# Optimization experiments

Measured on AMD Instinct MI355X. Metric: run time of the kernel, lower is better.

## Reference

```python
import jax, jax.numpy as jnp
import numpy as np

D = 512          # hidden_dim
H_HEADS = 8
DH = D // H_HEADS  # 64
L = 6            # n_layers
P = 8            # patch size
KT = 3           # temporal kernel
Z_DIM = 32
FILM_SCALE = 0.5
ROPE_BASE = 10000.0
EPS = 1e-5


def layer_norm(x, g, b):
    mu = x.mean(-1, keepdims=True)
    var = ((x - mu) ** 2).mean(-1, keepdims=True)
    return (x - mu) * jax.lax.rsqrt(var + EPS) * g + b


def rotate_half(x):
    x1, x2 = jnp.split(x, 2, axis=-1)
    return jnp.concatenate([-x2, x1], axis=-1)


def rope_time(T, dtype):
    half = DH // 2
    inv_freq = ROPE_BASE ** (-(jnp.arange(half, dtype=dtype) / half))  # (half,)
    angles = jnp.arange(T, dtype=dtype)[:, None] * inv_freq[None, :]   # (T, half)
    sin = jnp.concatenate([jnp.sin(angles), jnp.sin(angles)], -1)      # (T, DH)
    cos = jnp.concatenate([jnp.cos(angles), jnp.cos(angles)], -1)
    return sin, cos


def setup_inputs() -> dict:
    key = jax.random.key(0)
    ks = iter(jax.random.split(key, 64))
    n = lambda shape, s=0.02: jax.random.normal(next(ks), shape, jnp.float32) * s
    inp = {
        "x": jax.random.normal(next(ks), (16, 32, 3, 64, 64), jnp.float32),
        "z": jax.random.normal(next(ks), (16, 32, Z_DIM), jnp.float32),
        # tokenizer: CausalConv3d (kt,ph,pw)=(3,8,8), stride (1,8,8)
        "conv_w": n((D, 3, KT, P, P)),
        "conv_b": jnp.zeros((D,), jnp.float32),
        "tok_g": jnp.ones((D,), jnp.float32),
        "tok_b": jnp.zeros((D,), jnp.float32),
        # FiLM from z -> (gamma, beta)
        "film_w": n((Z_DIM, 2 * D)),
        "film_b": jnp.zeros((2 * D,), jnp.float32),
        # transformer blocks (stacked over L)
        "ln1_g": jnp.ones((L, D), jnp.float32), "ln1_b": jnp.zeros((L, D), jnp.float32),
        "kqv_w": n((L, D, 3 * D)), "kqv_b": jnp.zeros((L, 3 * D), jnp.float32),
        "proj_w": n((L, D, D)), "proj_b": jnp.zeros((L, D), jnp.float32),
        "ln2_g": jnp.ones((L, D), jnp.float32), "ln2_b": jnp.zeros((L, D), jnp.float32),
        "mlp_w1": n((L, D, 4 * D)), "mlp_b1": jnp.zeros((L, 4 * D), jnp.float32),
        "mlp_w2": n((L, 4 * D, D)), "mlp_b2": jnp.zeros((L, D), jnp.float32),
        "rs_attn": jnp.full((L,), 0.5, jnp.float32),
        "rs_mlp": jnp.full((L,), 0.5, jnp.float32),
        # scoring head
        "head_g": jnp.ones((D,), jnp.float32), "head_b": jnp.zeros((D,), jnp.float32),
        "head_w": n((D, 1)), "head_bias": jnp.zeros((1,), jnp.float32),
    }
    return inp


def _forward(x, z, conv_w, conv_b, tok_g, tok_b, film_w, film_b,
             ln1_g, ln1_b, kqv_w, kqv_b, proj_w, proj_b, ln2_g, ln2_b,
             mlp_w1, mlp_b1, mlp_w2, mlp_b2, rs_attn, rs_mlp,
             head_g, head_b, head_w, head_bias):
    B, T, C, Himg, Wimg = x.shape
    # ---- SpatialTemporalTokenizer: causal Conv3d (pad time on past only) ----
    xc = jnp.transpose(x, (0, 2, 1, 3, 4))  # [B,C,T,H,W]
    y = jax.lax.conv_general_dilated(
        xc, conv_w, window_strides=(1, P, P),
        padding=[(KT - 1, 0), (0, 0), (0, 0)],
        dimension_numbers=("NCDHW", "OIDHW", "NCDHW"))
    y = y + conv_b[None, :, None, None, None]          # [B,D,T,Hn,Wn]
    Hn, Wn = y.shape[3], y.shape[4]
    tok = jnp.transpose(y, (0, 2, 3, 4, 1)).reshape(B, T, Hn * Wn, D)
    tok = layer_norm(tok, tok_g, tok_b)                 # [B,T,N,D]
    # ---- FiLM conditioning from z ----
    gb = z @ film_w + film_b                            # [B,T,2D]
    gamma, beta = jnp.split(gb, 2, axis=-1)
    tok = (1.0 + FILM_SCALE * gamma)[:, :, None, :] * tok + (FILM_SCALE * beta)[:, :, None, :]
    # ---- spatial pooling -> temporal sequence ----
    h = tok.mean(axis=2)                                # [B,T,D]
    # ---- transformer stack (causal, time RoPE, pre-LN, gated residuals) ----
    sin_t, cos_t = rope_time(T, h.dtype)                # (T, DH)
    causal = jnp.tril(jnp.ones((T, T), bool))
    neg_inf = jnp.finfo(h.dtype).min
    for i in range(L):
        xi = layer_norm(h, ln1_g[i], ln1_b[i])
        kqv = xi @ kqv_w[i] + kqv_b[i]                  # [B,T,3D]
        k, q, v = jnp.split(kqv, 3, axis=-1)            # torch chunk order: k,q,v
        sh = lambda t: t.reshape(B, T, H_HEADS, DH).transpose(0, 2, 1, 3)  # [B,h,T,d]
        q, k, v = sh(q), sh(k), sh(v)
        q = q * cos_t + rotate_half(q) * sin_t
        k = k * cos_t + rotate_half(k) * sin_t
        att = jnp.einsum("bhqd,bhkd->bhqk", q, k) / np.sqrt(DH)
        att = jnp.where(causal[None, None], att, neg_inf)
        att = jax.nn.softmax(att, axis=-1)
        yv = jnp.einsum("bhqk,bhkd->bhqd", att, v)
        yv = yv.transpose(0, 2, 1, 3).reshape(B, T, D)
        attn_out = yv @ proj_w[i] + proj_b[i]
        h = h + rs_attn[i] * attn_out
        x2 = layer_norm(h, ln2_g[i], ln2_b[i])
        m = jax.nn.gelu(x2 @ mlp_w1[i] + mlp_b1[i], approximate=False) @ mlp_w2[i] + mlp_b2[i]
        h = h + rs_mlp[i] * m
    # ---- per-timestep score head ----
    h = layer_norm(h, head_g, head_b)
    score = (h @ head_w + head_bias)[..., 0]            # [B,T]
    return score


def reference(x, z, conv_w, conv_b, tok_g, tok_b, film_w, film_b,
              ln1_g, ln1_b, kqv_w, kqv_b, proj_w, proj_b, ln2_g, ln2_b,
              mlp_w1, mlp_b1, mlp_w2, mlp_b2, rs_attn, rs_mlp,
              head_g, head_b, head_w, head_bias):
    return _forward(x, z, conv_w, conv_b, tok_g, tok_b, film_w, film_b,
                    ln1_g, ln1_b, kqv_w, kqv_b, proj_w, proj_b, ln2_g, ln2_b,
                    mlp_w1, mlp_b1, mlp_w2, mlp_b2, rs_attn, rs_mlp,
                    head_g, head_b, head_w, head_bias)
```

## Files before the change

kernel.cpp:

```cpp
#include <hip/hip_runtime.h>
#include <math.h>

#define EPS 1e-5f

typedef __attribute__((ext_vector_type(8))) short short8;
typedef __attribute__((ext_vector_type(4))) float f32x4;

__device__ __forceinline__ short f2bf(float f) {
    unsigned u = __float_as_uint(f);
    u += 0x7fffu + ((u >> 16) & 1u);
    return (short)(u >> 16);
}
__device__ __forceinline__ float bf2f(short s) {
    return __uint_as_float(((unsigned)(unsigned short)s) << 16);
}
__device__ __forceinline__ void async16(const void* g, void* l) {
    __builtin_amdgcn_global_load_lds(
        (const __attribute__((address_space(1))) unsigned*)g,
        (__attribute__((address_space(3))) unsigned*)l, 16, 0, 0);
}

__device__ __forceinline__ float block_reduce_sum_256(float v, float* red) {
    #pragma unroll
    for (int o = 32; o > 0; o >>= 1) v += __shfl_down(v, o, 64);
    __syncthreads();
    if ((threadIdx.x & 63) == 0) red[threadIdx.x >> 6] = v;
    __syncthreads();
    return red[0] + red[1] + red[2] + red[3];
}

__global__ __launch_bounds__(256) void prep_misc(
    const float* __restrict__ z, const float* __restrict__ fw,
    const float* __restrict__ fb, float* __restrict__ gb,
    const float* __restrict__ conv_w, short* __restrict__ wbf,
    const float* __restrict__ x, short* __restrict__ xbf) {
    __shared__ float zs[32];
    int bi = blockIdx.x, tid = threadIdx.x;
    if (bi < 512) {
        if (tid < 32) zs[tid] = z[bi * 32 + tid];
        __syncthreads();
        for (int j = tid; j < 1024; j += 256) {
            float acc = fb[j];
            #pragma unroll
            for (int k = 0; k < 32; k++) acc = fmaf(zs[k], fw[k * 1024 + j], acc);
            gb[bi * 1024 + j] = acc;
        }
    } else if (bi < 1664) {
        int i = (bi - 512) * 256 + tid;
        wbf[i] = f2bf(conv_w[i]);
    } else {
        int i = (bi - 1664) * 256 + tid;
        float4 a = *(const float4*)(x + (size_t)i * 8);
        float4 b = *(const float4*)(x + (size_t)i * 8 + 4);
        short8 o = {f2bf(a.x), f2bf(a.y), f2bf(a.z), f2bf(a.w),
                    f2bf(b.x), f2bf(b.y), f2bf(b.z), f2bf(b.w)};
        *(short8*)(xbf + (size_t)i * 8) = o;
    }
}

__global__ __launch_bounds__(256) void prep_tcast(
    const float* __restrict__ kqv_w, short* __restrict__ kqvT,
    const float* __restrict__ proj_w, short* __restrict__ projT,
    const float* __restrict__ mlp_w1, short* __restrict__ mlp1T,
    const float* __restrict__ mlp_w2, short* __restrict__ mlp2T) {
    __shared__ float tile[32][33];
    int bi = blockIdx.x;
    const float* src; short* dst; int NT, K, N, rel;
    if (bi < 4608)       { src = kqv_w;  dst = kqvT;  NT = 48; K = 512;  N = 1536; rel = bi; }
    else if (bi < 6144)  { src = proj_w; dst = projT; NT = 16; K = 512;  N = 512;  rel = bi - 4608; }
    else if (bi < 12288) { src = mlp_w1; dst = mlp1T; NT = 64; K = 512;  N = 2048; rel = bi - 6144; }
    else                 { src = mlp_w2; dst = mlp2T; NT = 16; K = 2048; N = 512;  rel = bi - 12288; }
    int per = NT * (K / 32);
    int layer = rel / per, r2 = rel - layer * per;
    int nt = r2 % NT, kt = r2 / NT;
    src += (size_t)layer * K * N;
    dst += (size_t)layer * N * K;
    int n0 = nt * 32, k0 = kt * 32;
    int lx = threadIdx.x & 31, ly = threadIdx.x >> 5;
    #pragma unroll
    for (int i = 0; i < 32; i += 8)
        tile[ly + i][lx] = src[(size_t)(k0 + ly + i) * N + n0 + lx];
    __syncthreads();
    int kp = threadIdx.x & 15, nn = threadIdx.x >> 4;
    #pragma unroll
    for (int i = 0; i < 2; i++) {
        int row = nn + i * 16;
        short2 o = {f2bf(tile[kp * 2][row]), f2bf(tile[kp * 2 + 1][row])};
        *(short2*)(dst + (size_t)(n0 + row) * K + k0 + kp * 2) = o;
    }
}

__global__ __launch_bounds__(256, 2) void conv_fused(
    const short* __restrict__ xbf, const short* __restrict__ wbf,
    const float* __restrict__ cb, const float* __restrict__ tg,
    const float* __restrict__ tb, const float* __restrict__ gb,
    float* __restrict__ h) {
    __shared__ short As[64 * 32];
    __shared__ short Bs[512 * 32];
    __shared__ float redsum[4][64], redss[4][64];
    __shared__ float mu_s[64], inv_s[64];
    int bt = blockIdx.x, b = bt >> 5, t = bt & 31;
    int tid = threadIdx.x;
    int wave = tid >> 6, lane = tid & 63, quad = lane >> 4, l16 = lane & 15;

    int rowA = tid >> 2;
    int cA = (tid & 3) ^ ((rowA >> 1) & 3);
    int hn = rowA >> 3, wn2 = rowA & 7;
    long long baseA = (((long long)(b * 32 + t - 2) * 3) << 12)
                      + (long long)(hn * 8) * 64 + wn2 * 8;

    f32x4 acc[4][8];
    #pragma unroll
    for (int mt = 0; mt < 4; mt++)
        #pragma unroll
        for (int nt = 0; nt < 8; nt++) acc[mt][nt] = (f32x4){0.f, 0.f, 0.f, 0.f};

    for (int k0 = 0; k0 < 576; k0 += 32) {
        #pragma unroll
        for (int e = 0; e < 8; e++) {
            int s = e * 256 + tid;
            int n = s >> 2;
            int c = (s & 3) ^ ((n >> 1) & 3);
            async16(wbf + (size_t)n * 576 + k0 + c * 8, Bs + s * 8);
        }
        {
            int ks = (k0 >> 3) + cA;
            int ch = (ks >= 24) + (ks >= 48);
            int r = ks - ch * 24;
            int kt = r >> 3, ph = r & 7;
            short8 v8 = (short8){0, 0, 0, 0, 0, 0, 0, 0};
            if (t + kt >= 2)
                v8 = *(const short8*)(xbf + baseA
                        + ((long long)(kt * 3 + ch) << 12) + ph * 64);
            *(short8*)(As + tid * 8) = v8;
        }
        __syncthreads();
        short8 af[4], bf[8];
        #pragma unroll
        for (int mt = 0; mt < 4; mt++) {
            int row = mt * 16 + l16;
            int pc = quad ^ ((row >> 1) & 3);
            af[mt] = *(const short8*)(As + row * 32 + pc * 8);
        }
        #pragma unroll
        for (int nt = 0; nt < 8; nt++) {
            int row = wave * 128 + nt * 16 + l16;
            int pc = quad ^ ((row >> 1) & 3);
            bf[nt] = *(const short8*)(Bs + row * 32 + pc * 8);
        }
        #pragma unroll
        for (int mt = 0; mt < 4; mt++)
            #pragma unroll
            for (int nt = 0; nt < 8; nt++)
                acc[mt][nt] = __builtin_amdgcn_mfma_f32_16x16x32_bf16(
                    af[mt], bf[nt], acc[mt][nt], 0, 0, 0);
        __syncthreads();
    }

    float cbn[8], tgn[8], tbn[8], Gn[8], Ben[8];
    #pragma unroll
    for (int nt = 0; nt < 8; nt++) {
        int n = wave * 128 + nt * 16 + l16;
        cbn[nt] = cb[n]; tgn[nt] = tg[n]; tbn[nt] = tb[n];
        Gn[nt]  = 1.f + 0.5f * gb[bt * 1024 + n];
        Ben[nt] = 0.5f * gb[bt * 1024 + 512 + n];
    }
    #pragma unroll
    for (int mt = 0; mt < 4; mt++)
        #pragma unroll
        for (int reg = 0; reg < 4; reg++) {
            float s = 0.f, ss = 0.f;
            #pragma unroll
            for (int nt = 0; nt < 8; nt++) {
                float v = acc[mt][nt][reg] + cbn[nt];
                s += v; ss += v * v;
            }
            #pragma unroll
            for (int o = 1; o < 16; o <<= 1) {
                s  += __shfl_xor(s, o, 64);
                ss += __shfl_xor(ss, o, 64);
            }
            if (l16 == 0) {
                int m = mt * 16 + quad * 4 + reg;
                redsum[wave][m] = s; redss[wave][m] = ss;
            }
        }
    __syncthreads();
    if (tid < 64) {
        float S  = redsum[0][tid] + redsum[1][tid] + redsum[2][tid] + redsum[3][tid];
        float SS = redss[0][tid] + redss[1][tid] + redss[2][tid] + redss[3][tid];
        float mu = S * (1.f / 512.f);
        float var = SS * (1.f / 512.f) - mu * mu;
        mu_s[tid] = mu; inv_s[tid] = rsqrtf(var + EPS);
    }
    __syncthreads();
    float hacc[8] = {0.f, 0.f, 0.f, 0.f, 0.f, 0.f, 0.f, 0.f};
    #pragma unroll
    for (int mt = 0; mt < 4; mt++)
        #pragma unroll
        for (int reg = 0; reg < 4; reg++) {
            int m = mt * 16 + quad * 4 + reg;
            float mu = mu_s[m], inv = inv_s[m];
            #pragma unroll
            for (int nt = 0; nt < 8; nt++) {
                float v = acc[mt][nt][reg] + cbn[nt];
                hacc[nt] += (v - mu) * inv;
            }
        }
    #pragma unroll
    for (int nt = 0; nt < 8; nt++) {
        hacc[nt] += __shfl_xor(hacc[nt], 16, 64);
        hacc[nt] += __shfl_xor(hacc[nt], 32, 64);
    }
    if (quad == 0)
        #pragma unroll
        for (int nt = 0; nt < 8; nt++) {
            int n = wave * 128 + nt * 16 + l16;
            h[bt * 512 + n] = Gn[nt] * (tgn[nt] * (hacc[nt] * (1.f / 64.f)) + tbn[nt])
                              + Ben[nt];
        }
}

__global__ __launch_bounds__(256) void attn_fused(
    const float* __restrict__ hsrc, const float* __restrict__ lng,
    const float* __restrict__ lnb, const short* __restrict__ Bw,
    const float* __restrict__ bias, short* __restrict__ yv) {
    __shared__ char smem[57344] __attribute__((aligned(16)));
    __shared__ float mu_s[32], inv_s[32];
    short* As = (short*)smem;
    short* Bs = (short*)(smem + 32768);
    float (*qs)[64] = (float(*)[64])(smem);
    float (*ks)[64] = (float(*)[64])(smem + 8192);
    float (*vs)[64] = (float(*)[64])(smem + 16384);
    float (*qr)[64] = (float(*)[64])(smem + 24576);
    float (*kr)[64] = (float(*)[64])(smem + 32768);
    float (*att)[32] = (float(*)[32])(smem + 40960);
    int blk = blockIdx.x, b = blk >> 3, hh = blk & 7;
    int tid = threadIdx.x;
    int m0 = b * 32;
    {
        int row = tid >> 3, l8 = tid & 7;
        const float* hp = hsrc + (size_t)(m0 + row) * 512 + l8 * 64;
        float s = 0.f, ss = 0.f;
        #pragma unroll
        for (int i = 0; i < 16; i++) {
            float4 v = *(const float4*)(hp + i * 4);
            s += v.x + v.y + v.z + v.w;
            ss += v.x * v.x + v.y * v.y + v.z * v.z + v.w * v.w;
        }
        s += __shfl_xor(s, 1, 64); ss += __shfl_xor(ss, 1, 64);
        s += __shfl_xor(s, 2, 64); ss += __shfl_xor(ss, 2, 64);
        s += __shfl_xor(s, 4, 64); ss += __shfl_xor(ss, 4, 64);
        if (l8 == 0) {
            float mu = s * (1.f / 512.f);
            float var = ss * (1.f / 512.f) - mu * mu;
            mu_s[row] = mu;
            inv_s[row] = rsqrtf(var + EPS);
        }
    }
    __syncthreads();
    #pragma unroll
    for (int e = 0; e < 8; e++) {
        int lc = e * 256 + tid;
        int row = lc >> 6, cc = lc & 63;
        float mu = mu_s[row], inv = inv_s[row];
        const float* hp = hsrc + (size_t)(m0 + row) * 512 + cc * 8;
        float4 a = *(const float4*)hp, b2 = *(const float4*)(hp + 4);
        float4 g0 = *(const float4*)(lng + cc * 8), g1 = *(const float4*)(lng + cc * 8 + 4);
        float4 b0 = *(const float4*)(lnb + cc * 8), b1 = *(const float4*)(lnb + cc * 8 + 4);
        short8 o = {f2bf((a.x - mu) * inv * g0.x + b0.x),
                    f2bf((a.y - mu) * inv * g0.y + b0.y),
                    f2bf((a.z - mu) * inv * g0.z + b0.z),
                    f2bf((a.w - mu) * inv * g0.w + b0.w),
                    f2bf((b2.x - mu) * inv * g1.x + b1.x),
                    f2bf((b2.y - mu) * inv * g1.y + b1.y),
                    f2bf((b2.z - mu) * inv * g1.z + b1.z),
                    f2bf((b2.w - mu) * inv * g1.w + b1.w)};
        *(short8*)(As + (row * 64 + (cc ^ (row & 7))) * 8) = o;
    }
    __syncthreads();
    int wave = tid >> 6, lane = tid & 63, quad = lane >> 4, l16 = lane & 15;
    f32x4 acc[2][3];
    #pragma unroll
    for (int m2 = 0; m2 < 2; m2++)
        #pragma unroll
        for (int g = 0; g < 3; g++) acc[m2][g] = (f32x4){0.f, 0.f, 0.f, 0.f};
    for (int k0 = 0; k0 < 512; k0 += 64) {
        #pragma unroll
        for (int e = 0; e < 6; e++) {
            int p = e * 256 + tid;
            int row = p >> 3, seg = (p & 7) ^ (row & 7);
            int n = ((row >> 6) << 9) + hh * 64 + (row & 63);
            async16(Bw + (size_t)n * 512 + k0 + seg * 8, Bs + p * 8);
        }
        __syncthreads();
        #pragma unroll
        for (int ksub = 0; ksub < 2; ksub++) {
            int ccb = ksub * 4 + quad;
            short8 af[2], bf[3];
            #pragma unroll
            for (int m2 = 0; m2 < 2; m2++) {
                int row = m2 * 16 + l16;
                int cc = (k0 >> 3) + ccb;
                af[m2] = *(const short8*)(As + (row * 64 + (cc ^ (row & 7))) * 8);
            }
            #pragma unroll
            for (int g = 0; g < 3; g++) {
                int row = g * 64 + wave * 16 + l16;
                bf[g] = *(const short8*)(Bs + (row * 8 + (ccb ^ (row & 7))) * 8);
            }
            #pragma unroll
            for (int m2 = 0; m2 < 2; m2++)
                #pragma unroll
                for (int g = 0; g < 3; g++)
                    acc[m2][g] = __builtin_amdgcn_mfma_f32_16x16x32_bf16(
                        af[m2], bf[g], acc[m2][g], 0, 0, 0);
        }
        __syncthreads();
    }
    float bb0 = bias[hh * 64 + wave * 16 + l16];
    float bb1 = bias[512 + hh * 64 + wave * 16 + l16];
    float bb2 = bias[1024 + hh * 64 + wave * 16 + l16];
    int dcol = wave * 16 + l16;
    #pragma unroll
    for (int m2 = 0; m2 < 2; m2++)
        #pragma unroll
        for (int reg = 0; reg < 4; reg++) {
            int tkn = m2 * 16 + quad * 4 + reg;
            ks[tkn][dcol] = acc[m2][0][reg] + bb0;
            qs[tkn][dcol] = acc[m2][1][reg] + bb1;
            vs[tkn][dcol] = acc[m2][2][reg] + bb2;
        }
    __syncthreads();
    const float lnb_c = logf(10000.f) / 32.f;
    for (int idx = tid; idx < 2048; idx += 256) {
        int t = idx >> 6, d = idx & 63;
        int j = d & 31;
        float ang = (float)t * expf(-(float)j * lnb_c);
        float sv = sinf(ang), cv = cosf(ang);
        float qv = qs[t][d], kv = ks[t][d];
        float qo = qs[t][d ^ 32], ko = ks[t][d ^ 32];
        float rq = (d < 32) ? -qo : qo;
        float rk = (d < 32) ? -ko : ko;
        qr[t][d] = qv * cv + rq * sv;
        kr[t][d] = kv * cv + rk * sv;
    }
    __syncthreads();
    #pragma unroll
    for (int l = 0; l < 4; l++) {
        int idx = l * 256 + tid;
        int qt = idx >> 5, kt2 = idx & 31;
        float s;
        if (kt2 > qt) {
            s = -1e30f;
        } else {
            float a = 0.f;
            #pragma unroll
            for (int d = 0; d < 64; d++) a = fmaf(qr[qt][d], kr[kt2][d], a);
            s = a * 0.125f;
        }
        att[qt][kt2] = s;
    }
    __syncthreads();
    if (tid < 32) {
        float m = -1e30f;
        #pragma unroll
        for (int k = 0; k < 32; k++) m = fmaxf(m, att[tid][k]);
        float sum = 0.f;
        #pragma unroll
        for (int k = 0; k < 32; k++) {
            float e = expf(att[tid][k] - m);
            att[tid][k] = e;
            sum += e;
        }
        float inv = 1.f / sum;
        #pragma unroll
        for (int k = 0; k < 32; k++) att[tid][k] *= inv;
    }
    __syncthreads();
    for (int idx = tid; idx < 2048; idx += 256) {
        int t = idx >> 6, d = idx & 63;
        float a = 0.f;
        #pragma unroll
        for (int k = 0; k < 32; k++) a = fmaf(att[t][k], vs[k][d], a);
        yv[(size_t)(b * 32 + t) * 512 + hh * 64 + d] = f2bf(a);
    }
}

__global__ __launch_bounds__(256) void gemm_ln(
    const float* __restrict__ hsrc, const float* __restrict__ lng,
    const float* __restrict__ lnb, const short* __restrict__ Bw,
    const float* __restrict__ bias, int N, int mode,
    float* __restrict__ outf, short* __restrict__ outb) {
    __shared__ short As[32 * 512];
    __shared__ short Bs[128 * 128];
    __shared__ float mu_s[32], inv_s[32];
    int tid = threadIdx.x;
    int m0 = blockIdx.y * 32, n0 = blockIdx.x * 128;
    {
        int row = tid >> 3, l8 = tid & 7;
        const float* hp = hsrc + (size_t)(m0 + row) * 512 + l8 * 64;
        float s = 0.f, ss = 0.f;
        #pragma unroll
        for (int i = 0; i < 16; i++) {
            float4 v = *(const float4*)(hp + i * 4);
            s += v.x + v.y + v.z + v.w;
            ss += v.x * v.x + v.y * v.y + v.z * v.z + v.w * v.w;
        }
        s += __shfl_xor(s, 1, 64); ss += __shfl_xor(ss, 1, 64);
        s += __shfl_xor(s, 2, 64); ss += __shfl_xor(ss, 2, 64);
        s += __shfl_xor(s, 4, 64); ss += __shfl_xor(ss, 4, 64);
        if (l8 == 0) {
            float mu = s * (1.f / 512.f);
            float var = ss * (1.f / 512.f) - mu * mu;
            mu_s[row] = mu;
            inv_s[row] = rsqrtf(var + EPS);
        }
    }
    __syncthreads();
    #pragma unroll
    for (int e = 0; e < 8; e++) {
        int lc = e * 256 + tid;
        int row = lc >> 6, cc = lc & 63;
        float mu = mu_s[row], inv = inv_s[row];
        const float* hp = hsrc + (size_t)(m0 + row) * 512 + cc * 8;
        float4 a = *(const float4*)hp, b = *(const float4*)(hp + 4);
        float4 g0 = *(const float4*)(lng + cc * 8), g1 = *(const float4*)(lng + cc * 8 + 4);
        float4 b0 = *(const float4*)(lnb + cc * 8), b1 = *(const float4*)(lnb + cc * 8 + 4);
        short8 o = {f2bf((a.x - mu) * inv * g0.x + b0.x),
                    f2bf((a.y - mu) * inv * g0.y + b0.y),
                    f2bf((a.z - mu) * inv * g0.z + b0.z),
                    f2bf((a.w - mu) * inv * g0.w + b0.w),
                    f2bf((b.x - mu) * inv * g1.x + b1.x),
                    f2bf((b.y - mu) * inv * g1.y + b1.y),
                    f2bf((b.z - mu) * inv * g1.z + b1.z),
                    f2bf((b.w - mu) * inv * g1.w + b1.w)};
        *(short8*)(As + (row * 64 + (cc ^ (row & 7))) * 8) = o;
    }
    __syncthreads();
    int wave = tid >> 6, lane = tid & 63, quad = lane >> 4, l16 = lane & 15;
    f32x4 acc[2][2];
    #pragma unroll
    for (int a2 = 0; a2 < 2; a2++)
        #pragma unroll
        for (int b2 = 0; b2 < 2; b2++) acc[a2][b2] = (f32x4){0.f, 0.f, 0.f, 0.f};
    for (int k0 = 0; k0 < 512; k0 += 128) {
        #pragma unroll
        for (int e = 0; e < 8; e++) {
            int p = e * 256 + tid;
            int row = p >> 4, seg = (p & 15) ^ (row & 15);
            async16(Bw + (size_t)(n0 + row) * 512 + k0 + seg * 8, Bs + p * 8);
        }
        __syncthreads();
        #pragma unroll
        for (int ksub = 0; ksub < 4; ksub++) {
            int ccb = ksub * 4 + quad;
            short8 af[2], bf[2];
            #pragma unroll
            for (int m2 = 0; m2 < 2; m2++) {
                int row = m2 * 16 + l16;
                int cc = (k0 >> 3) + ccb;
                af[m2] = *(const short8*)(As + (row * 64 + (cc ^ (row & 7))) * 8);
            }
            #pragma unroll
            for (int n2 = 0; n2 < 2; n2++) {
                int row = wave * 32 + n2 * 16 + l16;
                bf[n2] = *(const short8*)(Bs + (row * 16 + (ccb ^ (row & 15))) * 8);
            }
            #pragma unroll
            for (int m2 = 0; m2 < 2; m2++)
                #pragma unroll
                for (int n2 = 0; n2 < 2; n2++)
                    acc[m2][n2] = __builtin_amdgcn_mfma_f32_16x16x32_bf16(
                        af[m2], bf[n2], acc[m2][n2], 0, 0, 0);
        }
        __syncthreads();
    }
    #pragma unroll
    for (int m2 = 0; m2 < 2; m2++)
        #pragma unroll
        for (int n2 = 0; n2 < 2; n2++)
            #pragma unroll
            for (int reg = 0; reg < 4; reg++) {
                int m = m0 + m2 * 16 + quad * 4 + reg;
                int n = n0 + wave * 32 + n2 * 16 + l16;
                float v = acc[m2][n2][reg] + bias[n];
                if (mode == 1) {
                    v = 0.5f * v * (1.f + erff(v * 0.70710678118f));
                    outb[(size_t)m * N + n] = f2bf(v);
                } else {
                    outf[(size_t)m * N + n] = v;
                }
            }
}

__global__ __launch_bounds__(256) void gemm_res(
    const short* __restrict__ Ag, const short* __restrict__ Bw,
    const float* __restrict__ bias, const float* __restrict__ rsPtr,
    float* __restrict__ hm, int K, int Ks) {
    __shared__ short As[32 * 128];
    __shared__ short Bs[64 * 128];
    int tid = threadIdx.x;
    int m0 = blockIdx.y * 32, n0 = blockIdx.x * 64;
    int kbase = blockIdx.z * Ks;
    int wave = tid >> 6, lane = tid & 63, quad = lane >> 4, l16 = lane & 15;
    f32x4 acc[2];
    acc[0] = (f32x4){0.f, 0.f, 0.f, 0.f};
    acc[1] = (f32x4){0.f, 0.f, 0.f, 0.f};
    for (int k0 = kbase; k0 < kbase + Ks; k0 += 128) {
        #pragma unroll
        for (int e = 0; e < 2; e++) {
            int p = e * 256 + tid;
            int row = p >> 4, seg = (p & 15) ^ (row & 15);
            async16(Ag + (size_t)(m0 + row) * K + k0 + seg * 8, As + p * 8);
        }
        #pragma unroll
        for (int e = 0; e < 4; e++) {
            int p = e * 256 + tid;
            int row = p >> 4, seg = (p & 15) ^ (row & 15);
            async16(Bw + (size_t)(n0 + row) * K + k0 + seg * 8, Bs + p * 8);
        }
        __syncthreads();
        #pragma unroll
        for (int ksub = 0; ksub < 4; ksub++) {
            int ccb = ksub * 4 + quad;
            short8 bf;
            {
                int row = wave * 16 + l16;
                bf = *(const short8*)(Bs + (row * 16 + (ccb ^ (row & 15))) * 8);
            }
            #pragma unroll
            for (int m2 = 0; m2 < 2; m2++) {
                int row = m2 * 16 + l16;
                short8 af = *(const short8*)(As + (row * 16 + (ccb ^ (row & 15))) * 8);
                acc[m2] = __builtin_amdgcn_mfma_f32_16x16x32_bf16(af, bf, acc[m2], 0, 0, 0);
            }
        }
        __syncthreads();
    }
    float rsv = *rsPtr;
    bool addb = (blockIdx.z == 0);
    #pragma unroll
    for (int m2 = 0; m2 < 2; m2++)
        #pragma unroll
        for (int reg = 0; reg < 4; reg++) {
            int m = m0 + m2 * 16 + quad * 4 + reg;
            int n = n0 + wave * 16 + l16;
            float v = acc[m2][reg] + (addb ? bias[n] : 0.f);
            atomicAdd(&hm[(size_t)m * 512 + n], rsv * v);
        }
}

__global__ __launch_bounds__(256) void head_kernel(
    const float* __restrict__ h, const float* __restrict__ g,
    const float* __restrict__ bb, const float* __restrict__ w,
    const float* __restrict__ bias0, float* __restrict__ out) {
    __shared__ float red[8];
    int token = blockIdx.x, tid = threadIdx.x;
    float v0 = h[token * 512 + tid], v1 = h[token * 512 + tid + 256];
    float s  = block_reduce_sum_256(v0 + v1, red);
    float ss = block_reduce_sum_256(v0 * v0 + v1 * v1, red);
    float mu = s * (1.f / 512.f);
    float var = ss * (1.f / 512.f) - mu * mu;
    float inv = rsqrtf(var + EPS);
    float n0 = (v0 - mu) * inv * g[tid] + bb[tid];
    float n1 = (v1 - mu) * inv * g[tid + 256] + bb[tid + 256];
    float dot = block_reduce_sum_256(n0 * w[tid] + n1 * w[tid + 256], red);
    if (tid == 0) out[token] = dot + bias0[0];
}

extern "C" void kernel_launch(void* const* d_in, const int* in_sizes, int n_in,
                              void* d_out, int out_size, void* d_ws, size_t ws_size,
                              hipStream_t stream) {
    const float* x       = (const float*)d_in[0];
    const float* z       = (const float*)d_in[1];
    const float* conv_w  = (const float*)d_in[2];
    const float* conv_b  = (const float*)d_in[3];
    const float* tok_g   = (const float*)d_in[4];
    const float* tok_b   = (const float*)d_in[5];
    const float* film_w  = (const float*)d_in[6];
    const float* film_b  = (const float*)d_in[7];
    const float* ln1_g   = (const float*)d_in[8];
    const float* ln1_b   = (const float*)d_in[9];
    const float* kqv_w   = (const float*)d_in[10];
    const float* kqv_b   = (const float*)d_in[11];
    const float* proj_w  = (const float*)d_in[12];
    const float* proj_b  = (const float*)d_in[13];
    const float* ln2_g   = (const float*)d_in[14];
    const float* ln2_b   = (const float*)d_in[15];
    const float* mlp_w1  = (const float*)d_in[16];
    const float* mlp_b1  = (const float*)d_in[17];
    const float* mlp_w2  = (const float*)d_in[18];
    const float* mlp_b2  = (const float*)d_in[19];
    const float* rs_attn = (const float*)d_in[20];
    const float* rs_mlp  = (const float*)d_in[21];
    const float* head_g  = (const float*)d_in[22];
    const float* head_b  = (const float*)d_in[23];
    const float* head_w  = (const float*)d_in[24];
    const float* head_bs = (const float*)d_in[25];
    float* out = (float*)d_out;

    float* ws = (float*)d_ws;
    float* gb   = ws;
    float* h    = gb + 524288;
    short* sb = (short*)(h + 262144);
    short* wbf   = sb;
    short* kqvT  = wbf   + 294912;
    short* projT = kqvT  + 4718592;
    short* mlp1T = projT + 1572864;
    short* mlp2T = mlp1T + 6291456;
    short* yvb   = mlp2T + 6291456;
    short* mbuf  = yvb   + 262144;
    short* xbf   = mbuf  + 1048576;

    prep_misc<<<4736, 256, 0, stream>>>(z, film_w, film_b, gb, conv_w, wbf, x, xbf);
    prep_tcast<<<18432, 256, 0, stream>>>(kqv_w, kqvT, proj_w, projT,
                                          mlp_w1, mlp1T, mlp_w2, mlp2T);

    conv_fused<<<512, 256, 0, stream>>>(xbf, wbf, conv_b, tok_g, tok_b, gb, h);

    for (int i = 0; i < 6; i++) {
        attn_fused<<<128, 256, 0, stream>>>(
            h, ln1_g + i * 512, ln1_b + i * 512,
            kqvT + (size_t)i * 1536 * 512, kqv_b + i * 1536, yvb);
        gemm_res<<<dim3(8, 16, 2), 256, 0, stream>>>(
            yvb, projT + (size_t)i * 512 * 512, proj_b + i * 512,
            rs_attn + i, h, 512, 256);
        gemm_ln<<<dim3(16, 16), 256, 0, stream>>>(
            h, ln2_g + i * 512, ln2_b + i * 512,
            mlp1T + (size_t)i * 2048 * 512, mlp_b1 + i * 2048,
            2048, 1, nullptr, mbuf);
        gemm_res<<<dim3(8, 16, 4), 256, 0, stream>>>(
            mbuf, mlp2T + (size_t)i * 512 * 2048, mlp_b2 + i * 512,
            rs_mlp + i, h, 2048, 512);
    }

    head_kernel<<<512, 256, 0, stream>>>(h, head_g, head_b, head_w, head_bs, out);
}
```

Measured before the change: 511.1 us.

## Use MFMA for attention scores and PV, precompute RoPE tables, merge prep kernels

Result: faster. 465.6 us (-8.9%).

```diff
diff --git a/kernel.cpp b/kernel.cpp
--- a/kernel.cpp
+++ b/kernel.cpp
@@ -29,14 +29,19 @@
     return red[0] + red[1] + red[2] + red[3];
 }
 
-__global__ __launch_bounds__(256) void prep_misc(
+__global__ __launch_bounds__(256) void prep_all(
     const float* __restrict__ z, const float* __restrict__ fw,
     const float* __restrict__ fb, float* __restrict__ gb,
     const float* __restrict__ conv_w, short* __restrict__ wbf,
-    const float* __restrict__ x, short* __restrict__ xbf) {
-    __shared__ float zs[32];
+    const float* __restrict__ x, short* __restrict__ xbf,
+    float* __restrict__ ropeS, float* __restrict__ ropeC,
+    const float* __restrict__ kqv_w, short* __restrict__ kqvT,
+    const float* __restrict__ proj_w, short* __restrict__ projT,
+    const float* __restrict__ mlp_w1, short* __restrict__ mlp1T,
+    const float* __restrict__ mlp_w2, short* __restrict__ mlp2T) {
     int bi = blockIdx.x, tid = threadIdx.x;
     if (bi < 512) {
+        __shared__ float zs[32];
         if (tid < 32) zs[tid] = z[bi * 32 + tid];
         __syncthreads();
         for (int j = tid; j < 1024; j += 256) {
@@ -45,43 +50,51 @@
             for (int k = 0; k < 32; k++) acc = fmaf(zs[k], fw[k * 1024 + j], acc);
             gb[bi * 1024 + j] = acc;
         }
-    } else if (bi < 1664) {
+        return;
+    }
+    if (bi < 1664) {
         int i = (bi - 512) * 256 + tid;
         wbf[i] = f2bf(conv_w[i]);
-    } else {
+        return;
+    }
+    if (bi < 4736) {
         int i = (bi - 1664) * 256 + tid;
         float4 a = *(const float4*)(x + (size_t)i * 8);
         float4 b = *(const float4*)(x + (size_t)i * 8 + 4);
         short8 o = {f2bf(a.x), f2bf(a.y), f2bf(a.z), f2bf(a.w),
                     f2bf(b.x), f2bf(b.y), f2bf(b.z), f2bf(b.w)};
         *(short8*)(xbf + (size_t)i * 8) = o;
-    }
-}
-
-__global__ __launch_bounds__(256) void prep_tcast(
-    const float* __restrict__ kqv_w, short* __restrict__ kqvT,
-    const float* __restrict__ proj_w, short* __restrict__ projT,
-    const float* __restrict__ mlp_w1, short* __restrict__ mlp1T,
-    const float* __restrict__ mlp_w2, short* __restrict__ mlp2T) {
+        return;
+    }
+    if (bi < 4740) {
+        int idx = (bi - 4736) * 256 + tid;
+        if (idx < 1024) {
+            int t = idx >> 5, j = idx & 31;
+            float ang = (float)t * expf(-(float)j * (logf(10000.f) / 32.f));
+            ropeS[idx] = sinf(ang);
+            ropeC[idx] = cosf(ang);
+        }
+        return;
+    }
     __shared__ float tile[32][33];
-    int bi = blockIdx.x;
+    int rel0 = bi - 4740;
     const float* src; short* dst; int NT, K, N, rel;
-    if (bi < 4608)       { src = kqv_w;  dst = kqvT;  NT = 48; K = 512;  N = 1536; rel = bi; }
-    else if (bi < 6144)  { src = proj_w; dst = projT; NT = 16; K = 512;  N = 512;  rel = bi - 4608; }
-    else if (bi < 12288) { src = mlp_w1; dst = mlp1T; NT = 64; K = 512;  N = 2048; rel = bi - 6144; }
-    else                 { src = mlp_w2; dst = mlp2T; NT = 16; K = 2048; N = 512;  rel = bi - 12288; }
+    if (rel0 < 4608)       { src = kqv_w;  dst = kqvT;  NT = 48; K = 512;  N = 1536; rel = rel0; }
+    else if (rel0 < 6144)  { src = proj_w; dst = projT; NT = 16; K = 512;  N = 512;  rel = rel0 - 4608; }
+    else if (rel0 < 12288) { src = mlp_w1; dst = mlp1T; NT = 64; K = 512;  N = 2048; rel = rel0 - 6144; }
+    else                   { src = mlp_w2; dst = mlp2T; NT = 16; K = 2048; N = 512;  rel = rel0 - 12288; }
     int per = NT * (K / 32);
     int layer = rel / per, r2 = rel - layer * per;
     int nt = r2 % NT, kt = r2 / NT;
     src += (size_t)layer * K * N;
     dst += (size_t)layer * N * K;
     int n0 = nt * 32, k0 = kt * 32;
-    int lx = threadIdx.x & 31, ly = threadIdx.x >> 5;
+    int lx = tid & 31, ly = tid >> 5;
     #pragma unroll
     for (int i = 0; i < 32; i += 8)
         tile[ly + i][lx] = src[(size_t)(k0 + ly + i) * N + n0 + lx];
     __syncthreads();
-    int kp = threadIdx.x & 15, nn = threadIdx.x >> 4;
+    int kp = tid & 15, nn = tid >> 4;
     #pragma unroll
     for (int i = 0; i < 2; i++) {
         int row = nn + i * 16;
@@ -224,17 +237,19 @@
 __global__ __launch_bounds__(256) void attn_fused(
     const float* __restrict__ hsrc, const float* __restrict__ lng,
     const float* __restrict__ lnb, const short* __restrict__ Bw,
-    const float* __restrict__ bias, short* __restrict__ yv) {
+    const float* __restrict__ bias, const float* __restrict__ ropeS,
+    const float* __restrict__ ropeC, short* __restrict__ yv) {
     __shared__ char smem[57344] __attribute__((aligned(16)));
     __shared__ float mu_s[32], inv_s[32];
     short* As = (short*)smem;
     short* Bs = (short*)(smem + 32768);
-    float (*qs)[64] = (float(*)[64])(smem);
-    float (*ks)[64] = (float(*)[64])(smem + 8192);
-    float (*vs)[64] = (float(*)[64])(smem + 16384);
-    float (*qr)[64] = (float(*)[64])(smem + 24576);
-    float (*kr)[64] = (float(*)[64])(smem + 32768);
-    float (*att)[32] = (float(*)[32])(smem + 40960);
+    float (*qsf)[64] = (float(*)[64])(smem);
+    float (*ksf)[64] = (float(*)[64])(smem + 8192);
+    short* vT  = (short*)(smem + 16384);
+    short* qrb = (short*)(smem + 20480);
+    short* krb = (short*)(smem + 24576);
+    float (*att)[33] = (float(*)[33])(smem + 28672);
+    short* pA  = (short*)(smem + 36864);
     int blk = blockIdx.x, b = blk >> 3, hh = blk & 7;
     int tid = threadIdx.x;
     int m0 = b * 32;
@@ -327,63 +342,82 @@
         #pragma unroll
         for (int reg = 0; reg < 4; reg++) {
             int tkn = m2 * 16 + quad * 4 + reg;
-            ks[tkn][dcol] = acc[m2][0][reg] + bb0;
-            qs[tkn][dcol] = acc[m2][1][reg] + bb1;
-            vs[tkn][dcol] = acc[m2][2][reg] + bb2;
-        }
-    __syncthreads();
-    const float lnb_c = logf(10000.f) / 32.f;
-    for (int idx = tid; idx < 2048; idx += 256) {
-        int t = idx >> 6, d = idx & 63;
-        int j = d & 31;
-        float ang = (float)t * expf(-(float)j * lnb_c);
-        float sv = sinf(ang), cv = cosf(ang);
-        float qv = qs[t][d], kv = ks[t][d];
-        float qo = qs[t][d ^ 32], ko = ks[t][d ^ 32];
+            ksf[tkn][dcol] = acc[m2][0][reg] + bb0;
+            qsf[tkn][dcol] = acc[m2][1][reg] + bb1;
+            vT[dcol * 32 + (((tkn >> 3) ^ (dcol & 3)) << 3) + (tkn & 7)]
+                = f2bf(acc[m2][2][reg] + bb2);
+        }
+    __syncthreads();
+    #pragma unroll
+    for (int e = 0; e < 8; e++) {
+        int idx = e * 256 + tid;
+        int t = idx >> 6, d = idx & 63, j = d & 31;
+        float sv = ropeS[t * 32 + j], cv = ropeC[t * 32 + j];
+        float qv = qsf[t][d], kv = ksf[t][d];
+        float qo = qsf[t][d ^ 32], ko = ksf[t][d ^ 32];
         float rq = (d < 32) ? -qo : qo;
         float rk = (d < 32) ? -ko : ko;
-        qr[t][d] = qv * cv + rq * sv;
-        kr[t][d] = kv * cv + rk * sv;
-    }
-    __syncthreads();
-    #pragma unroll
-    for (int l = 0; l < 4; l++) {
-        int idx = l * 256 + tid;
-        int qt = idx >> 5, kt2 = idx & 31;
-        float s;
-        if (kt2 > qt) {
-            s = -1e30f;
-        } else {
-            float a = 0.f;
-            #pragma unroll
-            for (int d = 0; d < 64; d++) a = fmaf(qr[qt][d], kr[kt2][d], a);
-            s = a * 0.125f;
-        }
-        att[qt][kt2] = s;
-    }
-    __syncthreads();
-    if (tid < 32) {
-        float m = -1e30f;
-        #pragma unroll
-        for (int k = 0; k < 32; k++) m = fmaxf(m, att[tid][k]);
-        float sum = 0.f;
-        #pragma unroll
-        for (int k = 0; k < 32; k++) {
-            float e = expf(att[tid][k] - m);
-            att[tid][k] = e;
-            sum += e;
-        }
-        float inv = 1.f / sum;
-        #pragma unroll
-        for (int k = 0; k < 32; k++) att[tid][k] *= inv;
-    }
-    __syncthreads();
-    for (int idx = tid; idx < 2048; idx += 256) {
-        int t = idx >> 6, d = idx & 63;
-        float a = 0.f;
-        #pragma unroll
-        for (int k = 0; k < 32; k++) a = fmaf(att[t][k], vs[k][d], a);
-        yv[(size_t)(b * 32 + t) * 512 + hh * 64 + d] = f2bf(a);
+        int addr = t * 64 + (((d >> 3) ^ (t & 7)) << 3) + (d & 7);
+        qrb[addr] = f2bf(qv * cv + rq * sv);
+        krb[addr] = f2bf(kv * cv + rk * sv);
+    }
+    __syncthreads();
+    int mw = wave & 1, nw = wave >> 1;
+    {
+        f32x4 sc = (f32x4){0.f, 0.f, 0.f, 0.f};
+        #pragma unroll
+        for (int kc = 0; kc < 2; kc++) {
+            int rq = mw * 16 + l16;
+            int rk = nw * 16 + l16;
+            short8 aq = *(const short8*)(qrb + rq * 64 + ((((kc << 2) + quad) ^ (rq & 7)) << 3));
+            short8 bk = *(const short8*)(krb + rk * 64 + ((((kc << 2) + quad) ^ (rk & 7)) << 3));
+            sc = __builtin_amdgcn_mfma_f32_16x16x32_bf16(aq, bk, sc, 0, 0, 0);
+        }
+        #pragma unroll
+        for (int reg = 0; reg < 4; reg++) {
+            int qt = mw * 16 + quad * 4 + reg;
+            int kt = nw * 16 + l16;
+            att[qt][kt] = (kt > qt) ? -1e30f : sc[reg] * 0.125f;
+        }
+    }
+    __syncthreads();
+    {
+        int row = tid >> 3, g = tid & 7;
+        float v0 = att[row][g * 4], v1 = att[row][g * 4 + 1];
+        float v2 = att[row][g * 4 + 2], v3 = att[row][g * 4 + 3];
+        float mx = fmaxf(fmaxf(v0, v1), fmaxf(v2, v3));
+        mx = fmaxf(mx, __shfl_xor(mx, 1, 64));
+        mx = fmaxf(mx, __shfl_xor(mx, 2, 64));
+        mx = fmaxf(mx, __shfl_xor(mx, 4, 64));
+        float e0 = expf(v0 - mx), e1 = expf(v1 - mx);
+        float e2 = expf(v2 - mx), e3 = expf(v3 - mx);
+        float s = e0 + e1 + e2 + e3;
+        s += __shfl_xor(s, 1, 64);
+        s += __shfl_xor(s, 2, 64);
+        s += __shfl_xor(s, 4, 64);
+        float inv = 1.f / s;
+        short* pp = pA + row * 32 + g * 4;
+        pp[0] = f2bf(e0 * inv); pp[1] = f2bf(e1 * inv);
+        pp[2] = f2bf(e2 * inv); pp[3] = f2bf(e3 * inv);
+    }
+    __syncthreads();
+    {
+        int rp = mw * 16 + l16;
+        short8 ap = *(const short8*)(pA + rp * 32 + quad * 8);
+        #pragma unroll
+        for (int i = 0; i < 2; i++) {
+            int nt = (wave >> 1) * 2 + i;
+            int rv = nt * 16 + l16;
+            short8 bv = *(const short8*)(vT + rv * 32 + (((quad ^ (rv & 3))) << 3));
+            f32x4 o = (f32x4){0.f, 0.f, 0.f, 0.f};
+            o = __builtin_amdgcn_mfma_f32_16x16x32_bf16(ap, bv, o, 0, 0, 0);
+            #pragma unroll
+            for (int reg = 0; reg < 4; reg++) {
+                int t = mw * 16 + quad * 4 + reg;
+                int d = nt * 16 + l16;
+                yv[(size_t)(b * 32 + t) * 512 + hh * 64 + d] = f2bf(o[reg]);
+            }
+        }
     }
 }
 
@@ -601,9 +635,11 @@
     float* out = (float*)d_out;
 
     float* ws = (float*)d_ws;
-    float* gb   = ws;
-    float* h    = gb + 524288;
-    short* sb = (short*)(h + 262144);
+    float* gb    = ws;
+    float* h     = gb + 524288;
+    float* ropeS = h + 262144;
+    float* ropeC = ropeS + 1024;
+    short* sb = (short*)(ropeC + 1024);
     short* wbf   = sb;
     short* kqvT  = wbf   + 294912;
     short* projT = kqvT  + 4718592;
@@ -613,16 +649,16 @@
     short* mbuf  = yvb   + 262144;
     short* xbf   = mbuf  + 1048576;
 
-    prep_misc<<<4736, 256, 0, stream>>>(z, film_w, film_b, gb, conv_w, wbf, x, xbf);
-    prep_tcast<<<18432, 256, 0, stream>>>(kqv_w, kqvT, proj_w, projT,
-                                          mlp_w1, mlp1T, mlp_w2, mlp2T);
+    prep_all<<<23172, 256, 0, stream>>>(
+        z, film_w, film_b, gb, conv_w, wbf, x, xbf, ropeS, ropeC,
+        kqv_w, kqvT, proj_w, projT, mlp_w1, mlp1T, mlp_w2, mlp2T);
 
     conv_fused<<<512, 256, 0, stream>>>(xbf, wbf, conv_b, tok_g, tok_b, gb, h);
 
     for (int i = 0; i < 6; i++) {
         attn_fused<<<128, 256, 0, stream>>>(
             h, ln1_g + i * 512, ln1_b + i * 512,
-            kqvT + (size_t)i * 1536 * 512, kqv_b + i * 1536, yvb);
+            kqvT + (size_t)i * 1536 * 512, kqv_b + i * 1536, ropeS, ropeC, yvb);
         gemm_res<<<dim3(8, 16, 2), 256, 0, stream>>>(
             yvb, projT + (size_t)i * 512 * 512, proj_b + i * 512,
             rs_attn + i, h, 512, 256);
```
